# Kernel optimization log

Hardware: AMD Instinct MI355X
Metric: run time of the kernel (lower is better)

## Reference

```python
import jax, jax.numpy as jnp
import numpy as np

NUM_GRAPHS = 1024
NODES_PER_GRAPH = 9
EDGES_PER_GRAPH = NODES_PER_GRAPH * (NODES_PER_GRAPH - 1)  # 72, fully connected no self-loops
N = NUM_GRAPHS * NODES_PER_GRAPH
E = NUM_GRAPHS * EDGES_PER_GRAPH
POS_DIM = 64
HID = 256          # gnn_hidden_dim / common_gnn_dim
S1_FEAT = HID      # stage1 feature_dim (after projection)
S1_INT = S1_FEAT + POS_DIM           # 320
S2_FEAT = 2 * HID                    # 512 (two scales concatenated)
S2_OUT = 2 * HID                     # 512
S2_INT = S2_FEAT + POS_DIM           # 576
LN_EPS = 1e-5
SM_EPS = 1e-16  # PyG softmax eps


def _dense(x, w, b):
    return x @ w + b


def _layer_norm(x, g, b):
    mu = jnp.mean(x, axis=-1, keepdims=True)
    var = jnp.mean(jnp.square(x - mu), axis=-1, keepdims=True)
    return (x - mu) * jax.lax.rsqrt(var + LN_EPS) * g + b


def _segment_softmax(logits, idx, n):
    # logits: [E,1]; normalize over edges sharing the same destination node
    m = jax.ops.segment_max(logits, idx, num_segments=n)
    e = jnp.exp(logits - m[idx])
    s = jax.ops.segment_sum(e, idx, num_segments=n)
    return e / (s[idx] + SM_EPS)


def _gnn_layer(x, pos, src, dst, n, p):
    # x: [N, F], pos: [N, P]; edges src->dst (PyG: edge_index[0]=src j, edge_index[1]=dst i)
    ix = jnp.concatenate([x, pos], axis=-1)            # integrated_x [N, F+P]
    ii, ij = ix[dst], ix[src]                          # integrated_x_i / _j per edge
    # pairwise_fn(integrated_x_j, integrated_x_i) -> mlp(cat([integrated_x_i, integrated_x_j]))
    pw_in = jnp.concatenate([ii, ij], axis=-1)         # [E, 2*(F+P)]
    rel = _dense(jax.nn.gelu(_dense(pw_in, p['pw1_w'], p['pw1_b']), approximate=False),
                 p['pw2_w'], p['pw2_b'])               # [E, out]
    att_in = jnp.concatenate([x[dst], x[src], pos[dst], pos[src]], axis=-1)
    logits = _dense(jax.nn.leaky_relu(_dense(att_in, p['att1_w'], p['att1_b']), 0.01),
                    p['att2_w'], p['att2_b'])          # [E, 1]
    attw = _segment_softmax(logits, dst, n)
    aggr = jax.ops.segment_sum(attw * rel, dst, num_segments=n)  # [N, out]
    upd = jax.nn.gelu(_dense(jnp.concatenate([ix, aggr], axis=-1), p['upd_w'], p['upd_b']),
                      approximate=False)
    h = _dense(ix, p['skip_w'], p['skip_b']) + upd
    return _layer_norm(h, p['ln_g'], p['ln_b'])


def _glorot(key, shape):
    fan_in, fan_out = shape[0], shape[1]
    lim = np.sqrt(6.0 / (fan_in + fan_out))
    return jax.random.uniform(key, shape, jnp.float32, -lim, lim)


def setup_inputs() -> dict:
    key = jax.random.key(0)
    ks = iter(jax.random.split(key, 64))

    feat_low = jax.random.normal(next(ks), (N, 512), jnp.float32)
    feat_high = jax.random.normal(next(ks), (N, 1024), jnp.float32)
    batch_indices = jnp.repeat(jnp.arange(NUM_GRAPHS), NODES_PER_GRAPH).astype(jnp.int32)

    # fully connected (no self loop) edges within each 9-node graph
    loc = np.array([(j, i) for i in range(NODES_PER_GRAPH) for j in range(NODES_PER_GRAPH) if i != j],
                   dtype=np.int64)  # (src, dst)
    off = np.repeat(np.arange(NUM_GRAPHS) * NODES_PER_GRAPH, EDGES_PER_GRAPH)
    src = np.tile(loc[:, 0], NUM_GRAPHS) + off
    dst = np.tile(loc[:, 1], NUM_GRAPHS) + off
    edge_index = jnp.asarray(np.stack([src, dst]), dtype=jnp.int32)  # [2, E]

    inp = dict(feat_low=feat_low, feat_high=feat_high,
               batch_indices=batch_indices, edge_index=edge_index)

    inp['pos_table'] = jax.random.normal(next(ks), (NODES_PER_GRAPH, POS_DIM), jnp.float32)
    inp['proj_low_w'] = _glorot(next(ks), (512, HID)); inp['proj_low_b'] = jnp.zeros((HID,), jnp.float32)
    inp['proj_high_w'] = _glorot(next(ks), (1024, HID)); inp['proj_high_b'] = jnp.zeros((HID,), jnp.float32)

    def layer_params(pref, fdim, pdim, out):
        integ = fdim + pdim
        d = {}
        d[pref + 'pw1_w'] = _glorot(next(ks), (2 * integ, out)); d[pref + 'pw1_b'] = jnp.zeros((out,), jnp.float32)
        d[pref + 'pw2_w'] = _glorot(next(ks), (out, out)); d[pref + 'pw2_b'] = jnp.zeros((out,), jnp.float32)
        d[pref + 'att1_w'] = _glorot(next(ks), (2 * fdim + 2 * pdim, out)); d[pref + 'att1_b'] = jnp.zeros((out,), jnp.float32)
        d[pref + 'att2_w'] = _glorot(next(ks), (out, 1)); d[pref + 'att2_b'] = jnp.zeros((1,), jnp.float32)
        d[pref + 'upd_w'] = _glorot(next(ks), (integ + out, out)); d[pref + 'upd_b'] = jnp.zeros((out,), jnp.float32)
        d[pref + 'ln_g'] = jnp.ones((out,), jnp.float32); d[pref + 'ln_b'] = jnp.zeros((out,), jnp.float32)
        d[pref + 'skip_w'] = _glorot(next(ks), (integ, out)); d[pref + 'skip_b'] = jnp.zeros((out,), jnp.float32)
        return d

    inp.update(layer_params('s1_', S1_FEAT, POS_DIM, HID))
    inp.update(layer_params('s2_', S2_FEAT, POS_DIM, S2_OUT))

    inp['cls1_w'] = _glorot(next(ks), (S2_OUT, HID)); inp['cls1_b'] = jnp.zeros((HID,), jnp.float32)
    inp['cls2_w'] = _glorot(next(ks), (HID, 1)); inp['cls2_b'] = jnp.zeros((1,), jnp.float32)
    return inp


def _forward(feat_low, feat_high, pos_table,
             proj_low_w, proj_low_b, proj_high_w, proj_high_b,
             s1, s2, cls1_w, cls1_b, cls2_w, cls2_b,
             batch_indices, edge_index):
    src, dst = edge_index[0], edge_index[1]
    pos_ids = jnp.tile(jnp.arange(NODES_PER_GRAPH), NUM_GRAPHS)
    pos = pos_table[pos_ids]                                  # [N, P]
    h_low = _gnn_layer(_dense(feat_low, proj_low_w, proj_low_b), pos, src, dst, N, s1)
    h_high = _gnn_layer(_dense(feat_high, proj_high_w, proj_high_b), pos, src, dst, N, s1)
    unified = jnp.concatenate([h_low, h_high], axis=-1)       # [N, 512]
    h2 = _gnn_layer(unified, pos, src, dst, N, s2)            # [N, 512]
    pooled = jax.ops.segment_sum(h2, batch_indices, num_segments=NUM_GRAPHS)
    hid = jax.nn.gelu(_dense(pooled, cls1_w, cls1_b), approximate=False)
    return _dense(hid, cls2_w, cls2_b)                        # [G, 1]


S1_KEYS = ['pw1_w', 'pw1_b', 'pw2_w', 'pw2_b', 'att1_w', 'att1_b', 'att2_w', 'att2_b',
           'upd_w', 'upd_b', 'ln_g', 'ln_b', 'skip_w', 'skip_b']


def reference(feat_low, feat_high, batch_indices, edge_index, pos_table,
              proj_low_w, proj_low_b, proj_high_w, proj_high_b,
              s1_pw1_w, s1_pw1_b, s1_pw2_w, s1_pw2_b, s1_att1_w, s1_att1_b,
              s1_att2_w, s1_att2_b, s1_upd_w, s1_upd_b, s1_ln_g, s1_ln_b,
              s1_skip_w, s1_skip_b,
              s2_pw1_w, s2_pw1_b, s2_pw2_w, s2_pw2_b, s2_att1_w, s2_att1_b,
              s2_att2_w, s2_att2_b, s2_upd_w, s2_upd_b, s2_ln_g, s2_ln_b,
              s2_skip_w, s2_skip_b,
              cls1_w, cls1_b, cls2_w, cls2_b):
    s1 = dict(zip(S1_KEYS, [s1_pw1_w, s1_pw1_b, s1_pw2_w, s1_pw2_b, s1_att1_w, s1_att1_b,
                            s1_att2_w, s1_att2_b, s1_upd_w, s1_upd_b, s1_ln_g, s1_ln_b,
                            s1_skip_w, s1_skip_b]))
    s2 = dict(zip(S1_KEYS, [s2_pw1_w, s2_pw1_b, s2_pw2_w, s2_pw2_b, s2_att1_w, s2_att1_b,
                            s2_att2_w, s2_att2_b, s2_upd_w, s2_upd_b, s2_ln_g, s2_ln_b,
                            s2_skip_w, s2_skip_b]))
    return _forward(feat_low, feat_high, pos_table,
                    proj_low_w, proj_low_b, proj_high_w, proj_high_b,
                    s1, s2, cls1_w, cls1_b, cls2_w, cls2_b,
                    batch_indices, edge_index)
```

## Files before the change

kernel.cpp:

```cpp
#include <hip/hip_runtime.h>
#include <math.h>

#define NUM_GRAPHS 1024
#define NPG 9
#define NN 9216
#define NN2 18432
#define POSD 64

typedef __attribute__((ext_vector_type(8))) short bf16x8;
typedef __attribute__((ext_vector_type(4))) float f32x4;

__device__ __forceinline__ float gelu_f(float x) {
    return 0.5f * x * (1.0f + erff(x * 0.70710678118654752f));
}
__device__ __forceinline__ float gelu_fast(float x) {
    float y = 0.7978845608f * x * (1.0f + 0.044715f * x * x);
    float t = __expf(-2.0f * fabsf(y));
    float r = (1.0f - t) / (1.0f + t);
    r = copysignf(r, y);
    return 0.5f * x * (1.0f + r);
}
__device__ __forceinline__ ushort f2b(float v) {
    unsigned u = __float_as_uint(v);
    return (ushort)((u + 0x7fffu + ((u >> 16) & 1u)) >> 16);
}
__device__ __forceinline__ float b2f(ushort u) {
    return __uint_as_float(((unsigned)u) << 16);
}
__device__ __forceinline__ void gload16(const ushort* g, ushort* l) {
    __builtin_amdgcn_global_load_lds((const __attribute__((address_space(1))) void*)g,
                                     (__attribute__((address_space(3))) void*)l, 16, 0, 0);
}

__global__ __launch_bounds__(256, 4) void mgemm(
    const ushort* __restrict__ A, int lda,
    const ushort* __restrict__ Wt, int ldw,
    const float* __restrict__ bias1,
    const float* __restrict__ prow, int ldp,
    float* outF, ushort* outB, int ldo,
    long partStride, int K)
{
    __shared__ ushort sA[2][128 * 32];
    __shared__ ushort sB[2][128 * 32];
    const int wv = threadIdx.x >> 6, lane = threadIdx.x & 63;
    const int rh = wv & 1, ch = wv >> 1;

    const int GX = gridDim.x;
    const int nwg = GX * gridDim.y;
    const int flat = blockIdx.y * GX + blockIdx.x;
    const int swq = nwg >> 3, swr = nwg & 7;
    const int xcd = flat & 7, posi = flat >> 3;
    const int tix = (xcd < swr ? xcd * (swq + 1) : swr * (swq + 1) + (xcd - swr) * swq) + posi;
    const int m0 = (tix / GX) * 128, n0 = (tix % GX) * 128;

    const int koff = blockIdx.z * K;

    f32x4 acc[4][4];
#pragma unroll
    for (int i = 0; i < 4; i++)
#pragma unroll
        for (int j = 0; j < 4; j++) acc[i][j] = (f32x4){0.f, 0.f, 0.f, 0.f};

    const ushort* Ab = A + (size_t)m0 * lda + koff;
    const ushort* Wb = Wt + (size_t)n0 * ldw + koff;
    if (outF) outF += (size_t)blockIdx.z * partStride;

    auto stage = [&](int b, int k0) {
#pragma unroll
        for (int i = 0; i < 2; i++) {
            int c = wv * 2 + i;
            int u = c * 64 + lane;
            int row = u >> 2, p = u & 3;
            int q = (p - (row >> 1)) & 3;
            gload16(Ab + (size_t)row * lda + k0 + q * 8, sA[b] + c * 512);
            gload16(Wb + (size_t)row * ldw + k0 + q * 8, sB[b] + c * 512);
        }
    };

    const int nsteps = K >> 5;
    stage(0, 0);
    int buf = 0;
    for (int s = 0; s < nsteps; s++) {
        __syncthreads();
        if (s + 1 < nsteps) stage(buf ^ 1, (s + 1) << 5);
        const int qg = lane >> 4;
        bf16x8 af[4], bfr[4];
#pragma unroll
        for (int bi = 0; bi < 4; bi++) {
            int r = rh * 64 + bi * 16 + (lane & 15);
            af[bi] = *(const bf16x8*)(sA[buf] + (r * 4 + ((qg + (r >> 1)) & 3)) * 8);
        }
#pragma unroll
        for (int bj = 0; bj < 4; bj++) {
            int r = ch * 64 + bj * 16 + (lane & 15);
            bfr[bj] = *(const bf16x8*)(sB[buf] + (r * 4 + ((qg + (r >> 1)) & 3)) * 8);
        }
#pragma unroll
        for (int bi = 0; bi < 4; bi++)
#pragma unroll
            for (int bj = 0; bj < 4; bj++)
                acc[bi][bj] = __builtin_amdgcn_mfma_f32_16x16x32_bf16(
                    af[bi], bfr[bj], acc[bi][bj], 0, 0, 0);
        buf ^= 1;
    }

    float* sP = (float*)sA;
    const bool haveP = (prow != 0);
    if (haveP) {
        __syncthreads();
        for (int i = threadIdx.x; i < 9 * 128; i += 256) {
            int rr = i >> 7, c = i & 127;
            sP[i] = prow[(size_t)rr * ldp + n0 + c] + bias1[n0 + c];
        }
        __syncthreads();
    }

#pragma unroll
    for (int bi = 0; bi < 4; bi++) {
#pragma unroll
        for (int r = 0; r < 4; r++) {
            int m = m0 + rh * 64 + bi * 16 + (lane >> 4) * 4 + r;
            int r9 = m % 9;
#pragma unroll
            for (int bj = 0; bj < 4; bj++) {
                int nc = ch * 64 + bj * 16 + (lane & 15);
                int n = n0 + nc;
                float v = acc[bi][bj][r];
                if (haveP) v += sP[r9 * 128 + nc];
                if (outF) outF[(size_t)m * ldo + n] = v;
                if (outB) outB[(size_t)m * ldo + n] = f2b(v);
            }
        }
    }
}

#define NJOBS 16
struct TJobsArg {
    const float* src[NJOBS];
    long dst[NJOBS];
    int K[NJOBS], N[NJOBS], off0[NJOBS], ldo[NJOBS];
};

__global__ __launch_bounds__(256) void tw_kernel(TJobsArg ja, ushort* wbuf)
{
    int j = blockIdx.y;
    int K = ja.K[j], N = ja.N[j];
    int tk = K >> 5, tn = N >> 5;
    int t = blockIdx.x;
    if (t >= tk * tn) return;
    int kt = t % tk, nt = t / tk;
    const float* src = ja.src[j];
    ushort* out = wbuf + ja.dst[j];
    int ldo = ja.ldo[j];
    __shared__ float L[32][33];
    int r = threadIdx.x >> 5, c = threadIdx.x & 31;
#pragma unroll
    for (int rr = 0; rr < 4; rr++) {
        int k = kt * 32 + rr * 8 + r;
        L[rr * 8 + r][c] = src[(size_t)(ja.off0[j] + k) * N + nt * 32 + c];
    }
    __syncthreads();
#pragma unroll
    for (int rr = 0; rr < 4; rr++) {
        int n = nt * 32 + rr * 8 + r;
        out[(size_t)n * ldo + kt * 32 + c] = f2b(L[c][rr * 8 + r]);
    }
}

__global__ void pjred_kernel(const float* __restrict__ PT,
                             const float* __restrict__ bl, const float* __restrict__ bh,
                             ushort* __restrict__ ixa1)
{
    int i = blockIdx.x * 256 + threadIdx.x;
    if (i >= NN2 * 64) return;
    int n = i >> 6, cq = i & 63;
    const float *p0, *p1, *bb; int r;
    if (n < NN) { p0 = PT; p1 = PT + (size_t)NN * 256; bb = bl; r = n; }
    else { p0 = PT + (size_t)2 * NN * 256; p1 = PT + (size_t)3 * NN * 256; bb = bh; r = n - NN; }
    float4 a = ((const float4*)(p0 + (size_t)r * 256))[cq];
    float4 b = ((const float4*)(p1 + (size_t)r * 256))[cq];
    float4 bs = ((const float4*)bb)[cq];
    ushort4 o;
    o.x = f2b(a.x + b.x + bs.x); o.y = f2b(a.y + b.y + bs.y);
    o.z = f2b(a.z + b.z + bs.z); o.w = f2b(a.w + b.w + bs.w);
    ((ushort4*)(ixa1 + (size_t)n * 512))[cq] = o;
}

__global__ __launch_bounds__(256) void edge_kernel(
    const ushort* __restrict__ PB, const float* __restrict__ att2_w,
    ushort* __restrict__ Gout, int ldG, float* __restrict__ S, int O, int cshift)
{
    __shared__ ushort sPB[9 * 2048];
    __shared__ float sAw[512];
    __shared__ float logits[72];
    __shared__ float aw[72];
    const int g = blockIdx.x;
    const int tid = threadIdx.x, lane = tid & 63, wave = tid >> 6;
    const int O4 = O * 4, O5 = O * 5;
    const int cpr = O >> 7;
    const int total = 9 * cpr;
    const ushort* gbase = PB + (size_t)g * 9 * O5;

    for (int i = wave; i < total; i += 4) {
        int row = i / cpr, co = i - row * cpr;
        gload16(gbase + (size_t)row * O5 + co * 512 + lane * 8, sPB + i * 512);
    }
    for (int c = tid; c < O; c += 256) sAw[c] = att2_w[c];
    __syncthreads();

    for (int e = wave; e < 72; e += 4) {
        int d = e >> 3, k = e & 7;
        int s = k + (k >= d);
        const ushort* ad = sPB + d * O4 + 2 * O;
        const ushort* as = sPB + s * O4 + 3 * O;
        float p = 0.f;
        for (int c0 = lane * 4; c0 < O; c0 += 256) {
            ushort4 a4 = *(const ushort4*)(ad + c0);
            ushort4 s4 = *(const ushort4*)(as + c0);
            const ushort* ap = (const ushort*)&a4;
            const ushort* sp = (const ushort*)&s4;
#pragma unroll
            for (int j = 0; j < 4; j++) {
                float v = b2f(ap[j]) + b2f(sp[j]);
                v = v > 0.f ? v : 0.01f * v;
                p += v * sAw[c0 + j];
            }
        }
#pragma unroll
        for (int off = 32; off; off >>= 1) p += __shfl_down(p, off, 64);
        if (lane == 0) logits[e] = p;
    }
    __syncthreads();

    if (tid < 9) {
        float m = -INFINITY;
#pragma unroll
        for (int k = 0; k < 8; k++) m = fmaxf(m, logits[tid * 8 + k]);
        float s = 0.f, ee[8];
#pragma unroll
        for (int k = 0; k < 8; k++) { ee[k] = expf(logits[tid * 8 + k] - m); s += ee[k]; }
        float inv = 1.0f / (s + 1e-16f);
#pragma unroll
        for (int k = 0; k < 8; k++) aw[tid * 8 + k] = ee[k] * inv;
        S[g * 9 + tid] = s * inv;
    }
    __syncthreads();

    const int nch = O >> 3;
    for (int idx = tid; idx < 9 * nch; idx += 256) {
        int n = idx >> cshift, cc = idx & (nch - 1);
        bf16x8 pdv = *(const bf16x8*)(sPB + n * O4 + cc * 8);
        const ushort* pp = (const ushort*)&pdv;
        float acc8[8];
#pragma unroll
        for (int j = 0; j < 8; j++) acc8[j] = 0.f;
#pragma unroll
        for (int k = 0; k < 8; k++) {
            int s = k + (k >= n);
            float w = aw[n * 8 + k];
            bf16x8 psv = *(const bf16x8*)(sPB + s * O4 + O + cc * 8);
            const ushort* qp = (const ushort*)&psv;
#pragma unroll
            for (int j = 0; j < 8; j++)
                acc8[j] += w * gelu_fast(b2f(pp[j]) + b2f(qp[j]));
        }
        ushort o8[8];
#pragma unroll
        for (int j = 0; j < 8; j++) o8[j] = f2b(acc8[j]);
        *(bf16x8*)(Gout + (size_t)(g * 9 + n) * ldG + cc * 8) = *(const bf16x8*)o8;
    }
}

__global__ __launch_bounds__(256) void ln_kernel(
    const float* __restrict__ P0, const float* __restrict__ P1,
    const float* __restrict__ ub, const float* __restrict__ vb,
    const float* __restrict__ S, const float* __restrict__ posU,
    const ushort* __restrict__ PBs, int ld5,
    const float* __restrict__ gw, const float* __restrict__ bw,
    ushort* outB, int ldoB, int rowsplit, float* outF, int O)
{
    __shared__ float sm[4];
    const int n = blockIdx.x, tid = threadIdx.x;
    const int lane = tid & 63, wid = tid >> 6;
    const float* p0 = P0 + (size_t)n * O;
    const float* p1 = P1 + (size_t)n * O;
    const ushort* sr = PBs + (size_t)n * ld5;
    const float* pu = posU + (size_t)(n % 9) * O;
    const float sv = S[n];
    const int cnt = O >> 8;

    float vals[2];
    float sum = 0.f;
#pragma unroll
    for (int i = 0; i < 2; i++) {
        if (i < cnt) {
            int c = tid + 256 * i;
            float t = p0[c] + p1[c] + ub[c] + vb[c] * sv + pu[c];
            vals[i] = gelu_f(t) + b2f(sr[c]);
            sum += vals[i];
        }
    }
#pragma unroll
    for (int off = 32; off; off >>= 1) sum += __shfl_down(sum, off, 64);
    if (lane == 0) sm[wid] = sum;
    __syncthreads();
    const float mu = (sm[0] + sm[1] + sm[2] + sm[3]) / (float)O;
    __syncthreads();

    float var = 0.f;
#pragma unroll
    for (int i = 0; i < 2; i++) {
        if (i < cnt) { float d = vals[i] - mu; var += d * d; }
    }
#pragma unroll
    for (int off = 32; off; off >>= 1) var += __shfl_down(var, off, 64);
    if (lane == 0) sm[wid] = var;
    __syncthreads();
    const float rstd = rsqrtf((sm[0] + sm[1] + sm[2] + sm[3]) / (float)O + 1e-5f);

    int orow = n, coloff = 0;
    if (n >= rowsplit) { orow = n - rowsplit; coloff = 256; }
#pragma unroll
    for (int i = 0; i < 2; i++) {
        if (i < cnt) {
            int c = tid + 256 * i;
            float v = (vals[i] - mu) * rstd * gw[c] + bw[c];
            if (outB) outB[(size_t)orow * ldoB + coloff + c] = f2b(v);
            if (outF) outF[(size_t)n * O + c] = v;
        }
    }
}

__global__ void prep_kernel(
    const float* __restrict__ pw1_b1, const float* __restrict__ att1_b1, const float* __restrict__ skip_b1,
    const float* __restrict__ pw1_b2, const float* __restrict__ att1_b2, const float* __restrict__ skip_b2,
    const float* __restrict__ pos_table,
    const float* __restrict__ s1_pw1, const float* __restrict__ s1_att, const float* __restrict__ s1_skp,
    const float* __restrict__ s2_pw1, const float* __restrict__ s2_att, const float* __restrict__ s2_skp,
    const float* __restrict__ pw2_b1, const float* __restrict__ upd_w1,
    const float* __restrict__ pw2_b2, const float* __restrict__ upd_w2,
    const float* __restrict__ pw2_w1, const float* __restrict__ pw2_w2,
    const float* __restrict__ feat_low, const float* __restrict__ feat_high,
    float* biasC1, float* biasC2,
    float* posPB1, float* posPB2, float* posU1, float* posU2,
    float* vb1, float* vb2, ushort* pw2f1, ushort* pw2f2, ushort* featB)
{
    int i = blockIdx.x * 256 + threadIdx.x;
    if (i < 1280) {
        float v;
        if (i < 256) v = pw1_b1[i];
        else if (i < 512) v = 0.f;
        else if (i < 768) v = att1_b1[i - 512];
        else if (i < 1024) v = 0.f;
        else v = skip_b1[i - 1024];
        biasC1[i] = v;
        return;
    }
    i -= 1280;
    if (i < 2560) {
        float v;
        if (i < 512) v = pw1_b2[i];
        else if (i < 1024) v = 0.f;
        else if (i < 1536) v = att1_b2[i - 1024];
        else if (i < 2048) v = 0.f;
        else v = skip_b2[i - 2048];
        biasC2[i] = v;
        return;
    }
    i -= 2560;
    if (i < 9 * 1280) {
        int r = i / 1280, n = i - r * 1280;
        int sec = n >> 8, c = n & 255;
        const float* src; int row0;
        if (sec == 0) { src = s1_pw1; row0 = 256; }
        else if (sec == 1) { src = s1_pw1; row0 = 576; }
        else if (sec == 2) { src = s1_att; row0 = 512; }
        else if (sec == 3) { src = s1_att; row0 = 576; }
        else { src = s1_skp; row0 = 256; }
        float a = 0.f;
        for (int k = 0; k < 64; k++) a += pos_table[r * 64 + k] * src[(size_t)(row0 + k) * 256 + c];
        posPB1[i] = a;
        return;
    }
    i -= 9 * 1280;
    if (i < 9 * 2560) {
        int r = i / 2560, n = i - r * 2560;
        int sec = n >> 9, c = n & 511;
        const float* src; int row0;
        if (sec == 0) { src = s2_pw1; row0 = 512; }
        else if (sec == 1) { src = s2_pw1; row0 = 1088; }
        else if (sec == 2) { src = s2_att; row0 = 1024; }
        else if (sec == 3) { src = s2_att; row0 = 1088; }
        else { src = s2_skp; row0 = 512; }
        float a = 0.f;
        for (int k = 0; k < 64; k++) a += pos_table[r * 64 + k] * src[(size_t)(row0 + k) * 512 + c];
        posPB2[i] = a;
        return;
    }
    i -= 9 * 2560;
    if (i < 9 * 256) {
        int r = i >> 8, c = i & 255;
        float a = 0.f;
        for (int k = 0; k < 64; k++) a += pos_table[r * 64 + k] * upd_w1[(size_t)(256 + k) * 256 + c];
        posU1[i] = a;
        return;
    }
    i -= 9 * 256;
    if (i < 9 * 512) {
        int r = i >> 9, c = i & 511;
        float a = 0.f;
        for (int k = 0; k < 64; k++) a += pos_table[r * 64 + k] * upd_w2[(size_t)(512 + k) * 512 + c];
        posU2[i] = a;
        return;
    }
    i -= 9 * 512;
    if (i < 256) {
        float a = 0.f;
        for (int j = 0; j < 256; j++) a += pw2_b1[j] * upd_w1[(size_t)(320 + j) * 256 + i];
        vb1[i] = a;
        return;
    }
    i -= 256;
    if (i < 512) {
        float a = 0.f;
        for (int j = 0; j < 512; j++) a += pw2_b2[j] * upd_w2[(size_t)(576 + j) * 512 + i];
        vb2[i] = a;
        return;
    }
    i -= 512;
    if (i < 256 * 256) { pw2f1[i] = f2b(pw2_w1[i]); return; }
    i -= 256 * 256;
    if (i < 512 * 512) { pw2f2[i] = f2b(pw2_w2[i]); return; }
    i -= 512 * 512;
    if (i < NN * 512 / 4) {
        float4 v = ((const float4*)feat_low)[i];
        ushort4 o;
        o.x = f2b(v.x); o.y = f2b(v.y); o.z = f2b(v.z); o.w = f2b(v.w);
        ((ushort4*)featB)[i] = o;
        return;
    }
    i -= NN * 512 / 4;
    if (i < NN * 1024 / 4) {
        float4 v = ((const float4*)feat_high)[i];
        ushort4 o;
        o.x = f2b(v.x); o.y = f2b(v.y); o.z = f2b(v.z); o.w = f2b(v.w);
        ((ushort4*)(featB + (size_t)NN * 512))[i] = o;
    }
}

__global__ __launch_bounds__(256) void head_kernel(
    const float* __restrict__ h2,
    const float* __restrict__ cls1_w, const float* __restrict__ cls1_b,
    const float* __restrict__ cls2_w, const float* __restrict__ cls2_b,
    float* __restrict__ out)
{
    __shared__ float pooled[4][512];
    __shared__ float hid[4][256];
    const int b = blockIdx.x, tid = threadIdx.x;

    for (int idx = tid; idx < 4 * 512; idx += 256) {
        int gi = idx >> 9, c = idx & 511;
        const float* base = h2 + (size_t)((b * 4 + gi) * 9) * 512 + c;
        float s = 0.f;
#pragma unroll
        for (int k = 0; k < NPG; k++) s += base[(size_t)k * 512];
        pooled[gi][c] = s;
    }
    __syncthreads();

    {
        float acc[4] = {0.f, 0.f, 0.f, 0.f};
        for (int c = 0; c < 512; c++) {
            float w = cls1_w[(size_t)c * 256 + tid];
#pragma unroll
            for (int gi = 0; gi < 4; gi++) acc[gi] += pooled[gi][c] * w;
        }
        float bb = cls1_b[tid];
#pragma unroll
        for (int gi = 0; gi < 4; gi++) hid[gi][tid] = gelu_f(acc[gi] + bb);
    }
    __syncthreads();

    {
        int gi = tid >> 6, lane = tid & 63;
        float p = 0.f;
#pragma unroll
        for (int i = 0; i < 4; i++) p += hid[gi][lane + 64 * i] * cls2_w[lane + 64 * i];
#pragma unroll
        for (int off = 32; off; off >>= 1) p += __shfl_down(p, off, 64);
        if (lane == 0) out[b * 4 + gi] = p + cls2_b[0];
    }
}

static inline void mg(hipStream_t st, int M, int N, int K,
                      const ushort* A, int lda, const ushort* Wt, int ldw,
                      const float* bias1, const float* prow, int ldp,
                      float* outF, ushort* outB, int ldo,
                      int nz, long partStride)
{
    dim3 grid(N / 128, M / 128, nz);
    mgemm<<<grid, dim3(256), 0, st>>>(A, lda, Wt, ldw, bias1, prow, ldp,
                                      outF, outB, ldo, partStride, K);
}

extern "C" void kernel_launch(void* const* d_in, const int* in_sizes, int n_in,
                              void* d_out, int out_size, void* d_ws, size_t ws_size,
                              hipStream_t stream)
{
    (void)in_sizes; (void)n_in; (void)out_size; (void)ws_size;
    const float* feat_low   = (const float*)d_in[0];
    const float* feat_high  = (const float*)d_in[1];
    const float* pos_table  = (const float*)d_in[4];
    const float* proj_low_w  = (const float*)d_in[5];
    const float* proj_low_b  = (const float*)d_in[6];
    const float* proj_high_w = (const float*)d_in[7];
    const float* proj_high_b = (const float*)d_in[8];
    const float* cls1_w = (const float*)d_in[37];
    const float* cls1_b = (const float*)d_in[38];
    const float* cls2_w = (const float*)d_in[39];
    const float* cls2_b = (const float*)d_in[40];
    float* out = (float*)d_out;

    const float* s1_pw1 = (const float*)d_in[9];
    const float* s1_att = (const float*)d_in[13];
    const float* s1_upd = (const float*)d_in[17];
    const float* s1_skp = (const float*)d_in[21];
    const float* s2_pw1 = (const float*)d_in[23];
    const float* s2_att = (const float*)d_in[27];
    const float* s2_upd = (const float*)d_in[31];
    const float* s2_skp = (const float*)d_in[35];

    const float* att2_w1 = (const float*)d_in[15];
    const float* upd_b1  = (const float*)d_in[18];
    const float* ln_g1   = (const float*)d_in[19];
    const float* ln_b1   = (const float*)d_in[20];
    const float* att2_w2 = (const float*)d_in[29];
    const float* upd_b2  = (const float*)d_in[32];
    const float* ln_g2   = (const float*)d_in[33];
    const float* ln_b2   = (const float*)d_in[34];

    char* base = (char*)d_ws;
    size_t cur = 0;
    auto alloc = [&](size_t bytes) { void* p = base + cur; cur += (bytes + 255) & ~(size_t)255; return p; };
    void*   PBreg = alloc((size_t)NN * 2560 * 2);
    ushort* PB    = (ushort*)PBreg;
    ushort* featB = (ushort*)PBreg;
    void*   IX1reg = alloc((size_t)NN2 * 512 * 2);
    ushort* ixa1  = (ushort*)IX1reg;
    float*  h2    = (float*)IX1reg;
    ushort* ixa2  = (ushort*)alloc((size_t)NN * 1024 * 2);
    float*  PT    = (float*)alloc((size_t)4 * NN * 256 * 4);
    float*  S     = (float*)alloc((size_t)NN2 * 4);
    float*  biasC1 = (float*)alloc(1280 * 4);
    float*  biasC2 = (float*)alloc(2560 * 4);
    float*  posPB1 = (float*)alloc(9 * 1280 * 4);
    float*  posPB2 = (float*)alloc(9 * 2560 * 4);
    float*  posU1  = (float*)alloc(9 * 256 * 4);
    float*  posU2  = (float*)alloc(9 * 512 * 4);
    float*  vb1   = (float*)alloc(256 * 4);
    float*  vb2   = (float*)alloc(512 * 4);
    ushort* wbuf  = (ushort*)alloc((size_t)3400000 * 2);

    TJobsArg ja;
    long woff[16];
    {
        struct J { const float* s; int K, N, off0, ldo; long sz; };
        J js[NJOBS] = {
            {proj_low_w,  512, 256, 0, 512, 512L * 256},
            {proj_high_w, 1024, 256, 0, 1024, 1024L * 256},
            {s1_pw1, 256, 256, 0, 256, 256L * 256},
            {s1_pw1, 256, 256, 320, 256, 256L * 256},
            {s1_att, 256, 256, 0, 256, 256L * 256},
            {s1_att, 256, 256, 256, 256, 256L * 256},
            {s1_skp, 256, 256, 0, 256, 256L * 256},
            {s1_upd, 256, 256, 0, 512, 512L * 256},
            {s1_upd, 256, 256, 320, 256, 256L * 256},
            {s2_pw1, 512, 512, 0, 512, 512L * 512},
            {s2_pw1, 512, 512, 576, 512, 512L * 512},
            {s2_att, 512, 512, 0, 512, 512L * 512},
            {s2_att, 512, 512, 512, 512, 512L * 512},
            {s2_skp, 512, 512, 0, 512, 512L * 512},
            {s2_upd, 512, 512, 0, 1024, 1024L * 512},
            {s2_upd, 512, 512, 576, 512, 512L * 512},
        };
        long off = 0;
        for (int i = 0; i < NJOBS; i++) {
            ja.src[i] = js[i].s; ja.K[i] = js[i].K; ja.N[i] = js[i].N;
            ja.off0[i] = js[i].off0; ja.ldo[i] = js[i].ldo;
            ja.dst[i] = off; woff[i] = off;
            off += js[i].sz;
        }
    }
    long pw2off1 = woff[15] + 512L * 512;
    long pw2off2 = pw2off1 + 256L * 256;
    tw_kernel<<<dim3(256, NJOBS), dim3(256), 0, stream>>>(ja, wbuf);

    ushort* wBig5_1 = wbuf + woff[2];
    ushort* updW1   = wbuf + woff[7];
    ushort* updbT1  = wbuf + woff[8];
    ushort* wBig5_2 = wbuf + woff[9];
    ushort* updW2   = wbuf + woff[14];
    ushort* updbT2  = wbuf + woff[15];
    ushort* pw2f1   = wbuf + pw2off1;
    ushort* pw2f2   = wbuf + pw2off2;

    {
        long tot = 1280 + 2560 + 9 * 1280 + 9 * 2560 + 9 * 256 + 9 * 512
                 + 256 + 512 + 256 * 256 + 512 * 512
                 + (long)NN * 512 / 4 + (long)NN * 1024 / 4;
        prep_kernel<<<dim3((unsigned)((tot + 255) / 256)), dim3(256), 0, stream>>>(
            (const float*)d_in[10], (const float*)d_in[14], (const float*)d_in[22],
            (const float*)d_in[24], (const float*)d_in[28], (const float*)d_in[36],
            pos_table,
            s1_pw1, s1_att, s1_skp, s2_pw1, s2_att, s2_skp,
            (const float*)d_in[12], s1_upd, (const float*)d_in[26], s2_upd,
            (const float*)d_in[11], (const float*)d_in[25],
            feat_low, feat_high,
            biasC1, biasC2, posPB1, posPB2, posU1, posU2, vb1, vb2, pw2f1, pw2f2, featB);
    }

    mg(stream, 256, 256, 256, updbT1, 256, pw2f1, 256, 0, 0, 0, 0, updW1 + 256, 512, 1, 0);
    mg(stream, 512, 512, 512, updbT2, 512, pw2f2, 512, 0, 0, 0, 0, updW2 + 512, 1024, 1, 0);

    mg(stream, NN, 256, 256, featB, 512, wbuf + woff[0], 512, 0, 0, 0,
       PT, 0, 256, 2, (long)NN * 256);
    mg(stream, NN, 256, 512, featB + (size_t)NN * 512, 1024, wbuf + woff[1], 1024, 0, 0, 0,
       PT + (size_t)2 * NN * 256, 0, 256, 2, (long)NN * 256);
    pjred_kernel<<<dim3(NN2 * 64 / 256), dim3(256), 0, stream>>>(PT, proj_low_b, proj_high_b, ixa1);

    mg(stream, NN2, 1280, 256, ixa1, 512, wBig5_1, 256, biasC1, posPB1, 1280, 0, PB, 1280, 1, 0);
    edge_kernel<<<dim3(2 * NUM_GRAPHS), dim3(256), 0, stream>>>(
        PB, att2_w1, ixa1 + 256, 512, S, 256, 5);
    mg(stream, NN2, 256, 256, ixa1, 512, updW1, 512, 0, 0, 0, PT, 0, 256, 2, (long)NN2 * 256);
    ln_kernel<<<dim3(NN2), dim3(256), 0, stream>>>(
        PT, PT + (size_t)NN2 * 256, upd_b1, vb1, S, posU1,
        PB + 4 * 256, 1280, ln_g1, ln_b1, ixa2, 1024, NN, 0, 256);

    mg(stream, NN, 2560, 512, ixa2, 1024, wBig5_2, 512, biasC2, posPB2, 2560, 0, PB, 2560, 1, 0);
    edge_kernel<<<dim3(NUM_GRAPHS), dim3(256), 0, stream>>>(
        PB, att2_w2, ixa2 + 512, 1024, S, 512, 6);
    mg(stream, NN, 512, 512, ixa2, 1024, updW2, 1024, 0, 0, 0, PT, 0, 512, 2, (long)NN * 512);
    ln_kernel<<<dim3(NN), dim3(256), 0, stream>>>(
        PT, PT + (size_t)NN * 512, upd_b2, vb2, S, posU2,
        PB + 4 * 512, 2560, ln_g2, ln_b2, 0, 0, 1 << 30, h2, 512);

    head_kernel<<<dim3(NUM_GRAPHS / 4), dim3(256), 0, stream>>>(h2, cls1_w, cls1_b, cls2_w, cls2_b, out);
}
```

Baseline: 562.9 us.

## Triple-buffer GEMM LDS staging with explicit vmcnt waits and MFMA priority

Converts the mgemm K-loop from a double-buffered to a triple-buffered LDS pipeline that prefetches two stages ahead. Explicit vmcnt waits and raw barriers replace __syncthreads, and s_setprio is raised around the MFMA block, all aimed at overlapping global loads with compute more fully. It also pads the bias/prow LDS table to a stride of 129 to avoid bank conflicts and uses nontemporal stores for bf16 output. The larger LDS footprint lowers occupancy from 4 to 3 workgroups per CU.

Result: slower. 585.3 us (+4.0%).

```diff
diff --git a/kernel.cpp b/kernel.cpp
--- a/kernel.cpp
+++ b/kernel.cpp
@@ -32,7 +32,7 @@
                                      (__attribute__((address_space(3))) void*)l, 16, 0, 0);
 }
 
-__global__ __launch_bounds__(256, 4) void mgemm(
+__global__ __launch_bounds__(256, 3) void mgemm(
     const ushort* __restrict__ A, int lda,
     const ushort* __restrict__ Wt, int ldw,
     const float* __restrict__ bias1,
@@ -40,8 +40,8 @@
     float* outF, ushort* outB, int ldo,
     long partStride, int K)
 {
-    __shared__ ushort sA[2][128 * 32];
-    __shared__ ushort sB[2][128 * 32];
+    __shared__ ushort sA[3][128 * 32];
+    __shared__ ushort sB[3][128 * 32];
     const int wv = threadIdx.x >> 6, lane = threadIdx.x & 63;
     const int rh = wv & 1, ch = wv >> 1;
 
@@ -79,29 +79,44 @@
 
     const int nsteps = K >> 5;
     stage(0, 0);
-    int buf = 0;
+    stage(1, 32);
+    int cur = 0;
     for (int s = 0; s < nsteps; s++) {
-        __syncthreads();
-        if (s + 1 < nsteps) stage(buf ^ 1, (s + 1) << 5);
+        if (s + 2 < nsteps) {
+            int nb = cur + 2; if (nb >= 3) nb -= 3;
+            stage(nb, (s + 2) << 5);
+            asm volatile("s_waitcnt vmcnt(8)" ::: "memory");
+        } else if (s + 2 == nsteps) {
+            asm volatile("s_waitcnt vmcnt(4)" ::: "memory");
+        } else {
+            asm volatile("s_waitcnt vmcnt(0)" ::: "memory");
+        }
+        __builtin_amdgcn_s_barrier();
+        __builtin_amdgcn_sched_barrier(0);
+
         const int qg = lane >> 4;
         bf16x8 af[4], bfr[4];
 #pragma unroll
         for (int bi = 0; bi < 4; bi++) {
             int r = rh * 64 + bi * 16 + (lane & 15);
-            af[bi] = *(const bf16x8*)(sA[buf] + (r * 4 + ((qg + (r >> 1)) & 3)) * 8);
+            af[bi] = *(const bf16x8*)(sA[cur] + (r * 4 + ((qg + (r >> 1)) & 3)) * 8);
         }
 #pragma unroll
         for (int bj = 0; bj < 4; bj++) {
             int r = ch * 64 + bj * 16 + (lane & 15);
-            bfr[bj] = *(const bf16x8*)(sB[buf] + (r * 4 + ((qg + (r >> 1)) & 3)) * 8);
-        }
+            bfr[bj] = *(const bf16x8*)(sB[cur] + (r * 4 + ((qg + (r >> 1)) & 3)) * 8);
+        }
+        __builtin_amdgcn_s_setprio(1);
 #pragma unroll
         for (int bi = 0; bi < 4; bi++)
 #pragma unroll
             for (int bj = 0; bj < 4; bj++)
                 acc[bi][bj] = __builtin_amdgcn_mfma_f32_16x16x32_bf16(
                     af[bi], bfr[bj], acc[bi][bj], 0, 0, 0);
-        buf ^= 1;
+        __builtin_amdgcn_s_setprio(0);
+        __builtin_amdgcn_sched_barrier(0);
+        __builtin_amdgcn_s_barrier();
+        cur++; if (cur >= 3) cur -= 3;
     }
 
     float* sP = (float*)sA;
@@ -110,7 +125,7 @@
         __syncthreads();
         for (int i = threadIdx.x; i < 9 * 128; i += 256) {
             int rr = i >> 7, c = i & 127;
-            sP[i] = prow[(size_t)rr * ldp + n0 + c] + bias1[n0 + c];
+            sP[rr * 129 + c] = prow[(size_t)rr * ldp + n0 + c] + bias1[n0 + c];
         }
         __syncthreads();
     }
@@ -126,9 +141,9 @@
                 int nc = ch * 64 + bj * 16 + (lane & 15);
                 int n = n0 + nc;
                 float v = acc[bi][bj][r];
-                if (haveP) v += sP[r9 * 128 + nc];
+                if (haveP) v += sP[r9 * 129 + nc];
                 if (outF) outF[(size_t)m * ldo + n] = v;
-                if (outB) outB[(size_t)m * ldo + n] = f2b(v);
+                if (outB) __builtin_nontemporal_store(f2b(v), outB + (size_t)m * ldo + n);
             }
         }
     }
```
